# Kernel optimization log

Measured on AMD Instinct MI355X. Metric: run time of the kernel, lower is better.

The kernel has to match this reference:

```python
import jax, jax.numpy as jnp
import numpy as np

RCR = 5.2          # radial cutoff
RCA = 3.5          # angular cutoff
ETA_R = 16.0
SHF_R = jnp.asarray(0.9 + 0.26875 * np.arange(16), jnp.float32)          # 16 radial shifts
ZETA = 32.0
SHF_Z = jnp.asarray((2 * np.arange(8) + 1) * np.pi / 16.0, jnp.float32)  # 8 angle shifts
ETA_A = 8.0
SHF_A = jnp.asarray(0.9 + 0.65 * np.arange(4), jnp.float32)              # 4 angular radial shifts
NUM_SPECIES = 4
NUM_PAIRS = NUM_SPECIES * (NUM_SPECIES + 1) // 2  # 10


def _pair_index_table():
    idx = np.zeros((NUM_SPECIES, NUM_SPECIES), np.int32)
    c = 0
    for s1 in range(NUM_SPECIES):
        for s2 in range(s1, NUM_SPECIES):
            idx[s1, s2] = c
            idx[s2, s1] = c
            c += 1
    return jnp.asarray(idx)

PAIR_IDX = _pair_index_table()


def _cutoff(d, rc):
    return jnp.where(d <= rc, 0.5 * jnp.cos(jnp.pi * d / rc) + 0.5, 0.0)


def setup_inputs() -> dict:
    key = jax.random.key(0)
    k1, k2 = jax.random.split(key)
    species = jax.random.randint(k1, (32, 48), 0, NUM_SPECIES, dtype=jnp.int32)
    coords = jax.random.uniform(k2, (32, 48, 3), jnp.float32) * 7.0  # 7 Angstrom box
    return {"species": species, "coords": coords}


def reference(species, coords):
    B, A = species.shape
    dt = coords.dtype
    # vec[b,i,j] = coords[j] - coords[i]
    diff = coords[:, None, :, :] - coords[:, :, None, :]           # [B,A,A,3]
    d2 = jnp.sum(diff * diff, -1)
    eye = jnp.eye(A, dtype=bool)
    dist = jnp.sqrt(jnp.where(eye, 1.0, d2))                        # safe on diagonal
    valid = (species[:, :, None] >= 0) & (species[:, None, :] >= 0) & (~eye)

    # ---------- radial AEV ----------
    fc_r = jnp.where(valid & (dist <= RCR), _cutoff(dist, RCR), 0.0)
    rad_terms = 0.25 * jnp.exp(-ETA_R * (dist[..., None] - SHF_R) ** 2) * fc_r[..., None]  # [B,A,A,16]
    sp_onehot = jax.nn.one_hot(jnp.clip(species, 0), NUM_SPECIES, dtype=dt)                # [B,A,4]
    radial = jnp.einsum('bijr,bjs->bisr', rad_terms, sp_onehot).reshape(B, A, NUM_SPECIES * 16)

    # ---------- angular AEV ----------
    in_ca = valid & (dist <= RCA)
    fc_a = jnp.where(in_ca, _cutoff(dist, RCA), 0.0)
    dotp = jnp.einsum('bijc,bikc->bijk', diff, diff)                # [B,A,A,A]
    cos_t = 0.95 * dotp / (dist[:, :, :, None] * dist[:, :, None, :])
    angles = jnp.arccos(cos_t)
    f1 = ((1.0 + jnp.cos(angles[..., None] - SHF_Z)) * 0.5) ** ZETA          # [B,A,A,A,8]
    avg_d = 0.5 * (dist[:, :, :, None] + dist[:, :, None, :])
    f2 = jnp.exp(-ETA_A * (avg_d[..., None] - SHF_A) ** 2)                   # [B,A,A,A,4]
    jk = jnp.triu(jnp.ones((A, A), bool), 1)                                 # unordered neighbor pairs j<k
    trip_mask = in_ca[:, :, :, None] & in_ca[:, :, None, :] & jk
    w = jnp.where(trip_mask, 2.0 * fc_a[:, :, :, None] * fc_a[:, :, None, :], 0.0)  # [B,A,A,A]
    pair_idx = PAIR_IDX[jnp.clip(species, 0)[:, :, None], jnp.clip(species, 0)[:, None, :]]  # [B,A,A]
    pair_oh = jax.nn.one_hot(pair_idx, NUM_PAIRS, dtype=dt)                  # [B,A,A,10]
    angular = jnp.einsum('bijk,bijka,bijkz,bjkp->bipaz', w, f2, f1, pair_oh)
    angular = angular.reshape(B, A, NUM_PAIRS * 4 * 8)

    aevs = jnp.concatenate([radial, angular], axis=-1)   # [B,A,384]
    return species, aevs
```

## Files before the change

kernel.cpp:

```cpp
#include <hip/hip_runtime.h>
#include <math.h>

#define NB 32
#define NA 48
#define RCRf 5.2f
#define RCAf 3.5f
#define PI_F 3.14159265358979f
#define CMAX 1000

typedef unsigned short ushort_t;
typedef __fp16 h2f __attribute__((ext_vector_type(2)));
static __device__ __forceinline__ unsigned pkh(float a, float b) {
    h2f v = __builtin_amdgcn_cvt_pkrtz(a, b);
    return __builtin_bit_cast(unsigned, v);
}
static __device__ __forceinline__ float uph(ushort_t u) {
    return (float)__builtin_bit_cast(__fp16, u);
}

static __device__ __forceinline__ void tri_decode(int t, int m, int T, int& jj, int& kk) {
    const int u = T - 1 - t;
    int r = (int)((sqrtf(8.0f * (float)u + 1.0f) - 1.0f) * 0.5f);
    while (r * (r + 1) / 2 > u) --r;
    while ((r + 1) * (r + 2) / 2 <= u) ++r;
    jj = m - 2 - r;
    kk = m - 1 - (u - r * (r + 1) / 2);
}

__global__ __launch_bounds__(320)
void aev_kernel(const int* __restrict__ species, const float* __restrict__ coords,
                float* __restrict__ out)
{
    const int bid = blockIdx.x;
    const int b = bid / NA;
    const int i = bid - b * NA;
    const int tid = threadIdx.x;

    __shared__ float pd[NA], pfr[NA];
    __shared__ int   ssp[NA];
    __shared__ __align__(16) float4 cpk[NA];
    __shared__ float cfc[NA];
    __shared__ int   csp[NA];
    __shared__ int   sm;
    __shared__ float radpart[5 * 64];
    __shared__ __align__(16) ushort_t f1h[CMAX * 8];
    __shared__ __align__(16) ushort_t w2h[CMAX * 4];
    __shared__ int   cnt[10];
    __shared__ unsigned cur[10];

    if (tid >= 256 && tid < 266) cnt[tid - 256] = 0;

    if (tid < 64) {
        const int j = tid;
        float dx = 0.f, dy = 0.f, dz = 0.f, d = 1.0f, fr = 0.0f, fa = 0.0f;
        int sj = 0;
        bool inA = false;
        if (j < NA) {
            const float* cb = coords + (size_t)b * NA * 3;
            const float xi = cb[3 * i], yi = cb[3 * i + 1], zi = cb[3 * i + 2];
            dx = cb[3 * j] - xi; dy = cb[3 * j + 1] - yi; dz = cb[3 * j + 2] - zi;
            d = sqrtf(dx * dx + dy * dy + dz * dz);
            sj = species[b * NA + j];
            if (j != i && d <= RCRf) fr = 0.5f * __cosf((PI_F / RCRf) * d) + 0.5f;
            if (j != i && d <= RCAf) { inA = true; fa = 0.5f * __cosf((PI_F / RCAf) * d) + 0.5f; }
            pd[j] = d; pfr[j] = fr; ssp[j] = sj;
        }
        const unsigned long long mask = __ballot(inA);
        if (inA) {
            const int pos = (int)__popcll(mask & ((1ull << j) - 1ull));
            cpk[pos] = make_float4(dx, dy, dz, d);
            cfc[pos] = fa; csp[pos] = sj;
        }
        if (j == 0) sm = (int)__popcll(mask);
    }
    __syncthreads();

    const int m = sm;
    const int T = m * (m - 1) / 2;
    const int nchunks = (T + CMAX - 1) / CMAX;

    {
        const int f = tid & 63, seg = tid >> 6;
        const int s = f >> 4, r = f & 15;
        const float shf = 0.9f + 0.26875f * (float)r;
        float acc = 0.0f;
        const int j0 = seg * 10, j1 = min(NA, j0 + 10);
        for (int j = j0; j < j1; ++j) {
            const float fr = pfr[j];
            if (fr != 0.0f) {
                const float u = pd[j] - shf;
                const float v = 0.25f * __expf(-16.0f * u * u) * fr;
                acc += (ssp[j] == s) ? v : 0.0f;
            }
        }
        radpart[seg * 64 + f] = acc;
    }
    {
        const int cT = min(CMAX, T);
        for (int t = tid; t < cT; t += 320) {
            int jj, kk; tri_decode(t, m, T, jj, kk);
            const int s1 = csp[jj], s2 = csp[kk];
            const int lo = min(s1, s2), hi = max(s1, s2);
            const int p = (lo * (9 - lo)) / 2 + (hi - lo);
            atomicAdd(&cnt[p], 1);
        }
    }
    __syncthreads();

    const int pmine = tid >> 5, amine = (tid >> 3) & 3, zmine = tid & 7;
    const float CZ[8] = { 0.98078528f, 0.83146961f, 0.55557023f, 0.19509032f,
                         -0.19509032f,-0.55557023f,-0.83146961f,-0.98078528f };
    const float SZ[8] = { 0.19509032f, 0.55557023f, 0.83146961f, 0.98078528f,
                          0.98078528f, 0.83146961f, 0.55557023f, 0.19509032f };
    const float SA[4] = { 0.9f, 1.55f, 2.2f, 2.85f };
    float acc_a = 0.0f;

    for (int c = 0; c < nchunks; ++c) {
        const int t0 = c * CMAX;
        const int cT = min(CMAX, T - t0);

        int mybase = 0, mycnt = 0, run = 0;
        #pragma unroll
        for (int p = 0; p < 10; ++p) {
            const int cp = cnt[p];
            if (p == pmine) { mybase = run; mycnt = cp; }
            if (tid < 10 && p == tid) cur[tid] = (unsigned)run;
            run += cp;
        }
        __syncthreads();

        for (int t = tid; t < cT; t += 320) {
            int jj, kk; tri_decode(t0 + t, m, T, jj, kk);
            const float4 qj = cpk[jj];
            const float4 qk = cpk[kk];
            const float dot = qj.x * qk.x + qj.y * qk.y + qj.z * qk.z;
            const float cosT = 0.95f * dot * __frcp_rn(qj.w * qk.w);
            const float sinT = sqrtf(fmaxf(1.0f - cosT * cosT, 0.0f));
            const float avg = 0.5f * (qj.w + qk.w);
            const float w = 2.0f * cfc[jj] * cfc[kk];
            const int s1 = csp[jj], s2 = csp[kk];
            const int lo = min(s1, s2), hi = max(s1, s2);
            const int p = (lo * (9 - lo)) / 2 + (hi - lo);

            float f1v[8];
            #pragma unroll
            for (int z = 0; z < 8; ++z) {
                const float base = 0.5f + 0.5f * (cosT * CZ[z] + sinT * SZ[z]);
                const float b2 = base * base, b4 = b2 * b2, b8 = b4 * b4, b16 = b8 * b8;
                f1v[z] = b16 * b16;
            }
            float w2v[4];
            #pragma unroll
            for (int a = 0; a < 4; ++a) {
                const float u = avg - SA[a];
                w2v[a] = w * __expf(-8.0f * u * u);
            }
            const unsigned pos = atomicAdd(&cur[p], 1u);
            uint4 rf;
            rf.x = pkh(f1v[0], f1v[1]); rf.y = pkh(f1v[2], f1v[3]);
            rf.z = pkh(f1v[4], f1v[5]); rf.w = pkh(f1v[6], f1v[7]);
            ((uint4*)f1h)[pos] = rf;
            uint2 rw;
            rw.x = pkh(w2v[0], w2v[1]); rw.y = pkh(w2v[2], w2v[3]);
            ((uint2*)w2h)[pos] = rw;
        }
        __syncthreads();

        for (int k = mybase; k < mybase + mycnt; ++k)
            acc_a += uph(w2h[k * 4 + amine]) * uph(f1h[k * 8 + zmine]);

        if (c + 1 < nchunks) {
            __syncthreads();
            if (tid < 10) cnt[tid] = 0;
            __syncthreads();
            const int n0 = (c + 1) * CMAX;
            const int nT = min(CMAX, T - n0);
            for (int t = tid; t < nT; t += 320) {
                int jj, kk; tri_decode(n0 + t, m, T, jj, kk);
                const int s1 = csp[jj], s2 = csp[kk];
                const int lo = min(s1, s2), hi = max(s1, s2);
                const int p = (lo * (9 - lo)) / 2 + (hi - lo);
                atomicAdd(&cnt[p], 1);
            }
            __syncthreads();
        }
    }

    float* op = out + NB * NA + (size_t)(b * NA + i) * 384;
    if (tid < 64) {
        op[tid] = radpart[tid] + radpart[64 + tid] + radpart[128 + tid] +
                  radpart[192 + tid] + radpart[256 + tid];
    }
    op[64 + tid] = acc_a;
    if (tid == 0) out[b * NA + i] = (float)ssp[i];
}

extern "C" void kernel_launch(void* const* d_in, const int* in_sizes, int n_in,
                              void* d_out, int out_size, void* d_ws, size_t ws_size,
                              hipStream_t stream) {
    const int*   species = (const int*)d_in[0];
    const float* coords  = (const float*)d_in[1];
    float*       out     = (float*)d_out;
    aev_kernel<<<NB * NA, 320, 0, stream>>>(species, coords, out);
}
```

Measured before the change: 65.89 us.

## Sort angular neighbors by species to compute pair buckets analytically

Neighbors within the angular cutoff are compacted in species order using per-species ballots, so each species-pair bucket's offset and count follow in closed form from the per-species counts. This removes the counting pass with shared atomics, the atomic slot allocation, and the extra barriers between them. Each triplet's output slot is now computed deterministically from its local indices. When there are several chunks, every chunk rescans all triplets and filters by position, which adds redundant decode work. Fast hardware sqrt and reciprocal builtins also replace the IEEE-accurate versions.

After: 64.18 us. -2.6%, faster.

```diff
diff --git a/kernel.cpp b/kernel.cpp
--- a/kernel.cpp
+++ b/kernel.cpp
@@ -20,7 +20,7 @@
 
 static __device__ __forceinline__ void tri_decode(int t, int m, int T, int& jj, int& kk) {
     const int u = T - 1 - t;
-    int r = (int)((sqrtf(8.0f * (float)u + 1.0f) - 1.0f) * 0.5f);
+    int r = (int)((__builtin_amdgcn_sqrtf(8.0f * (float)u + 1.0f) - 1.0f) * 0.5f);
     while (r * (r + 1) / 2 > u) --r;
     while ((r + 1) * (r + 2) / 2 <= u) ++r;
     jj = m - 2 - r;
@@ -40,15 +40,12 @@
     __shared__ int   ssp[NA];
     __shared__ __align__(16) float4 cpk[NA];
     __shared__ float cfc[NA];
-    __shared__ int   csp[NA];
-    __shared__ int   sm;
     __shared__ float radpart[5 * 64];
     __shared__ __align__(16) ushort_t f1h[CMAX * 8];
     __shared__ __align__(16) ushort_t w2h[CMAX * 4];
-    __shared__ int   cnt[10];
-    __shared__ unsigned cur[10];
-
-    if (tid >= 256 && tid < 266) cnt[tid - 256] = 0;
+    __shared__ int shb[11];
+    __shared__ int shn[4];
+    __shared__ int shs[3];
 
     if (tid < 64) {
         const int j = tid;
@@ -65,19 +62,40 @@
             if (j != i && d <= RCAf) { inA = true; fa = 0.5f * __cosf((PI_F / RCAf) * d) + 0.5f; }
             pd[j] = d; pfr[j] = fr; ssp[j] = sj;
         }
-        const unsigned long long mask = __ballot(inA);
+        const unsigned long long mk0 = __ballot(inA && sj == 0);
+        const unsigned long long mk1 = __ballot(inA && sj == 1);
+        const unsigned long long mk2 = __ballot(inA && sj == 2);
+        const unsigned long long mk3 = __ballot(inA && sj == 3);
+        const int n0 = (int)__popcll(mk0), n1 = (int)__popcll(mk1);
+        const int n2 = (int)__popcll(mk2), n3 = (int)__popcll(mk3);
         if (inA) {
-            const int pos = (int)__popcll(mask & ((1ull << j) - 1ull));
+            const unsigned long long below = (1ull << j) - 1ull;
+            int pos;
+            if (sj == 0)      pos = (int)__popcll(mk0 & below);
+            else if (sj == 1) pos = n0 + (int)__popcll(mk1 & below);
+            else if (sj == 2) pos = n0 + n1 + (int)__popcll(mk2 & below);
+            else              pos = n0 + n1 + n2 + (int)__popcll(mk3 & below);
             cpk[pos] = make_float4(dx, dy, dz, d);
-            cfc[pos] = fa; csp[pos] = sj;
-        }
-        if (j == 0) sm = (int)__popcll(mask);
+            cfc[pos] = fa;
+        }
+        if (j == 0) {
+            shn[0] = n0; shn[1] = n1; shn[2] = n2; shn[3] = n3;
+            shs[0] = n0; shs[1] = n0 + n1; shs[2] = n0 + n1 + n2;
+            const int c[10] = { n0*(n0-1)/2, n0*n1, n0*n2, n0*n3,
+                                n1*(n1-1)/2, n1*n2, n1*n3,
+                                n2*(n2-1)/2, n2*n3, n3*(n3-1)/2 };
+            int run = 0;
+            #pragma unroll
+            for (int p = 0; p < 10; ++p) { shb[p] = run; run += c[p]; }
+            shb[10] = run;
+        }
     }
     __syncthreads();
 
-    const int m = sm;
+    const int n0c = shn[0], n1c = shn[1], n2c = shn[2], n3c = shn[3];
+    const int m = n0c + n1c + n2c + n3c;
     const int T = m * (m - 1) / 2;
-    const int nchunks = (T + CMAX - 1) / CMAX;
+    const int ss1 = shs[0], ss2 = shs[1], ss3 = shs[2];
 
     {
         const int f = tid & 63, seg = tid >> 6;
@@ -95,19 +113,10 @@
         }
         radpart[seg * 64 + f] = acc;
     }
-    {
-        const int cT = min(CMAX, T);
-        for (int t = tid; t < cT; t += 320) {
-            int jj, kk; tri_decode(t, m, T, jj, kk);
-            const int s1 = csp[jj], s2 = csp[kk];
-            const int lo = min(s1, s2), hi = max(s1, s2);
-            const int p = (lo * (9 - lo)) / 2 + (hi - lo);
-            atomicAdd(&cnt[p], 1);
-        }
-    }
-    __syncthreads();
 
     const int pmine = tid >> 5, amine = (tid >> 3) & 3, zmine = tid & 7;
+    const int mybase = shb[pmine];
+    const int myend  = shb[pmine + 1];
     const float CZ[8] = { 0.98078528f, 0.83146961f, 0.55557023f, 0.19509032f,
                          -0.19509032f,-0.55557023f,-0.83146961f,-0.98078528f };
     const float SZ[8] = { 0.19509032f, 0.55557023f, 0.83146961f, 0.98078528f,
@@ -115,75 +124,62 @@
     const float SA[4] = { 0.9f, 1.55f, 2.2f, 2.85f };
     float acc_a = 0.0f;
 
+    const int nchunks = max(1, (T + CMAX - 1) / CMAX);
+
     for (int c = 0; c < nchunks; ++c) {
-        const int t0 = c * CMAX;
-        const int cT = min(CMAX, T - t0);
-
-        int mybase = 0, mycnt = 0, run = 0;
-        #pragma unroll
-        for (int p = 0; p < 10; ++p) {
-            const int cp = cnt[p];
-            if (p == pmine) { mybase = run; mycnt = cp; }
-            if (tid < 10 && p == tid) cur[tid] = (unsigned)run;
-            run += cp;
+        if (c) __syncthreads();
+        const int lo = c * CMAX;
+        const int hi = min(T, lo + CMAX);
+
+        for (int t = tid; t < T; t += 320) {
+            int jj, kk; tri_decode(t, m, T, jj, kk);
+            const int s1 = (jj >= ss1) + (jj >= ss2) + (jj >= ss3);
+            const int s2 = (kk >= ss1) + (kk >= ss2) + (kk >= ss3);
+            const int p  = (s1 * (9 - s1)) / 2 + (s2 - s1);
+            const int sb1 = s1 == 0 ? 0 : (s1 == 1 ? ss1 : (s1 == 2 ? ss2 : ss3));
+            const int sb2 = s2 == 0 ? 0 : (s2 == 1 ? ss1 : (s2 == 2 ? ss2 : ss3));
+            const int ns2 = s2 == 0 ? n0c : (s2 == 1 ? n1c : (s2 == 2 ? n2c : n3c));
+            const int jl = jj - sb1, kl = kk - sb2;
+            const int idx = (s1 == s2) ? ((jl * (2 * ns2 - jl - 1)) / 2 + (kl - jl - 1))
+                                       : (jl * ns2 + kl);
+            const int pos = shb[p] + idx;
+            if (pos >= lo && pos < hi) {
+                const float4 qj = cpk[jj];
+                const float4 qk = cpk[kk];
+                const float dot = qj.x * qk.x + qj.y * qk.y + qj.z * qk.z;
+                const float cosT = 0.95f * dot * __builtin_amdgcn_rcpf(qj.w * qk.w);
+                const float sinT = __builtin_amdgcn_sqrtf(fmaxf(1.0f - cosT * cosT, 0.0f));
+                const float avg = 0.5f * (qj.w + qk.w);
+                const float w = 2.0f * cfc[jj] * cfc[kk];
+
+                float f1v[8];
+                #pragma unroll
+                for (int z = 0; z < 8; ++z) {
+                    const float base = 0.5f + 0.5f * (cosT * CZ[z] + sinT * SZ[z]);
+                    const float b2 = base * base, b4 = b2 * b2, b8 = b4 * b4, b16 = b8 * b8;
+                    f1v[z] = b16 * b16;
+                }
+                float w2v[4];
+                #pragma unroll
+                for (int a = 0; a < 4; ++a) {
+                    const float u = avg - SA[a];
+                    w2v[a] = w * __expf(-8.0f * u * u);
+                }
+                const int wp = pos - lo;
+                uint4 rf;
+                rf.x = pkh(f1v[0], f1v[1]); rf.y = pkh(f1v[2], f1v[3]);
+                rf.z = pkh(f1v[4], f1v[5]); rf.w = pkh(f1v[6], f1v[7]);
+                ((uint4*)f1h)[wp] = rf;
+                uint2 rw;
+                rw.x = pkh(w2v[0], w2v[1]); rw.y = pkh(w2v[2], w2v[3]);
+                ((uint2*)w2h)[wp] = rw;
+            }
         }
         __syncthreads();
 
-        for (int t = tid; t < cT; t += 320) {
-            int jj, kk; tri_decode(t0 + t, m, T, jj, kk);
-            const float4 qj = cpk[jj];
-            const float4 qk = cpk[kk];
-            const float dot = qj.x * qk.x + qj.y * qk.y + qj.z * qk.z;
-            const float cosT = 0.95f * dot * __frcp_rn(qj.w * qk.w);
-            const float sinT = sqrtf(fmaxf(1.0f - cosT * cosT, 0.0f));
-            const float avg = 0.5f * (qj.w + qk.w);
-            const float w = 2.0f * cfc[jj] * cfc[kk];
-            const int s1 = csp[jj], s2 = csp[kk];
-            const int lo = min(s1, s2), hi = max(s1, s2);
-            const int p = (lo * (9 - lo)) / 2 + (hi - lo);
-
-            float f1v[8];
-            #pragma unroll
-            for (int z = 0; z < 8; ++z) {
-                const float base = 0.5f + 0.5f * (cosT * CZ[z] + sinT * SZ[z]);
-                const float b2 = base * base, b4 = b2 * b2, b8 = b4 * b4, b16 = b8 * b8;
-                f1v[z] = b16 * b16;
-            }
-            float w2v[4];
-            #pragma unroll
-            for (int a = 0; a < 4; ++a) {
-                const float u = avg - SA[a];
-                w2v[a] = w * __expf(-8.0f * u * u);
-            }
-            const unsigned pos = atomicAdd(&cur[p], 1u);
-            uint4 rf;
-            rf.x = pkh(f1v[0], f1v[1]); rf.y = pkh(f1v[2], f1v[3]);
-            rf.z = pkh(f1v[4], f1v[5]); rf.w = pkh(f1v[6], f1v[7]);
-            ((uint4*)f1h)[pos] = rf;
-            uint2 rw;
-            rw.x = pkh(w2v[0], w2v[1]); rw.y = pkh(w2v[2], w2v[3]);
-            ((uint2*)w2h)[pos] = rw;
-        }
-        __syncthreads();
-
-        for (int k = mybase; k < mybase + mycnt; ++k)
-            acc_a += uph(w2h[k * 4 + amine]) * uph(f1h[k * 8 + zmine]);
-
-        if (c + 1 < nchunks) {
-            __syncthreads();
-            if (tid < 10) cnt[tid] = 0;
-            __syncthreads();
-            const int n0 = (c + 1) * CMAX;
-            const int nT = min(CMAX, T - n0);
-            for (int t = tid; t < nT; t += 320) {
-                int jj, kk; tri_decode(n0 + t, m, T, jj, kk);
-                const int s1 = csp[jj], s2 = csp[kk];
-                const int lo = min(s1, s2), hi = max(s1, s2);
-                const int p = (lo * (9 - lo)) / 2 + (hi - lo);
-                atomicAdd(&cnt[p], 1);
-            }
-            __syncthreads();
-        }
+        const int k0 = max(mybase, lo), k1 = min(myend, hi);
+        for (int k = k0; k < k1; ++k)
+            acc_a += uph(w2h[(k - lo) * 4 + amine]) * uph(f1h[(k - lo) * 8 + zmine]);
     }
 
     float* op = out + NB * NA + (size_t)(b * NA + i) * 384;
```
